# Kernel optimization log

Hardware: AMD Instinct MI355X
Metric: run time of the kernel (lower is better)

## Reference

```python
import jax, jax.numpy as jnp
import numpy as np

IN_CAPS, IN_SIZE = 1152, 8
OUT_CAPS, OUT_SIZE = 10, 16
NUM_ITERS = 3


def squash(s, axis=-1, eps=1e-8):
    sq = jnp.sum(s * s, axis=axis, keepdims=True)
    norm = jnp.sqrt(sq + eps)
    return (sq / (1.0 + sq)) * (s / norm)


def setup_inputs() -> dict:
    key = jax.random.key(0)
    kx, kw = jax.random.split(key)
    x = jax.random.normal(kx, (512, IN_CAPS, IN_SIZE), dtype=jnp.float32)
    W = jax.random.normal(kw, (IN_CAPS, OUT_CAPS, OUT_SIZE, IN_SIZE), dtype=jnp.float32)
    return {"x": x, "W": W}


def reference(x, W):
    # u_hat[b,i,o,p] = sum_q W[i,o,p,q] x[b,i,q]   -> [B, I, O, P]
    u_hat = jnp.einsum("iopq,biq->biop", W, x)
    b_ij = jnp.zeros((IN_CAPS, OUT_CAPS), dtype=u_hat.dtype)
    v_j = None
    for _ in range(NUM_ITERS):
        # legacy F.softmax on [1,I,O,1] with no dim -> softmax over dim=1 (in_capsules)
        c_ij = jax.nn.softmax(b_ij, axis=0)                      # [I, O]
        s_j = jnp.einsum("io,biop->bop", c_ij, u_hat)            # [B, O, P]
        v_j = squash(s_j, axis=-1)                               # [B, O, P]
        # agreement, averaged over batch
        u_vj1 = jnp.einsum("biop,bop->io", u_hat, v_j) / x.shape[0]
        b_ij = b_ij + u_vj1
    return v_j  # [B, 10, 16]
```

## Files before the change

kernel.cpp:

```cpp
#include <hip/hip_runtime.h>
#include <hip/hip_bf16.h>

#define B 512
#define IC 1152
#define QD 8
#define OD 10
#define PD 16
#define KD (IC * QD)
#define NKB (KD / 32)
#define NCS 72
#define KSTEPS (NKB / NCS)
#define NCB 4
#define SOP (B * OD * PD)
#define IO (IC * OD)
#define XE (B * KD)
#define PREPX (XE / 8 / 256)

typedef short bf16x8 __attribute__((ext_vector_type(8)));
typedef short bf16x4 __attribute__((ext_vector_type(4)));
typedef float f32x4 __attribute__((ext_vector_type(4)));

__device__ __forceinline__ short f2bf(float f) {
  union { float f; unsigned u; } x;
  x.f = f;
  unsigned r = x.u + 0x7FFFu + ((x.u >> 16) & 1u);
  return (short)(r >> 16);
}

__global__ __launch_bounds__(256) void prep_kernel(const float* __restrict__ x,
                                                   const float* __restrict__ W,
                                                   float* __restrict__ bijT,
                                                   short* __restrict__ Bs,
                                                   short* __restrict__ xB) {
  const int bid = blockIdx.x, tid = threadIdx.x;
  if (bid < PREPX) {
    const size_t e0 = (((size_t)bid << 8) + tid) * 8;
    const float4 a = *(const float4*)(x + e0);
    const float4 b = *(const float4*)(x + e0 + 4);
    short ov[8];
    ov[0] = f2bf(a.x); ov[1] = f2bf(a.y); ov[2] = f2bf(a.z); ov[3] = f2bf(a.w);
    ov[4] = f2bf(b.x); ov[5] = f2bf(b.y); ov[6] = f2bf(b.z); ov[7] = f2bf(b.w);
    *(int4*)(xB + e0) = *(const int4*)ov;
    return;
  }
  const int t = (bid - PREPX) * 256 + tid;
  if (t < IO) bijT[t] = 0.f;
  const int kb = t / 160, n = t % 160;
  const int o = n >> 4, p = n & 15;
  const float ci = 1.0f / (float)IC;
  short ov[32];
#pragma unroll
  for (int quad = 0; quad < 4; ++quad) {
    const int i = kb * 4 + quad;
    const float4* wp = (const float4*)(W + (((size_t)i * OD + o) * PD + p) * QD);
    const float4 w0 = wp[0], w1 = wp[1];
    ov[quad * 8 + 0] = f2bf(ci * w0.x); ov[quad * 8 + 1] = f2bf(ci * w0.y);
    ov[quad * 8 + 2] = f2bf(ci * w0.z); ov[quad * 8 + 3] = f2bf(ci * w0.w);
    ov[quad * 8 + 4] = f2bf(ci * w1.x); ov[quad * 8 + 5] = f2bf(ci * w1.y);
    ov[quad * 8 + 6] = f2bf(ci * w1.z); ov[quad * 8 + 7] = f2bf(ci * w1.w);
  }
  int4* dst = (int4*)(Bs + (size_t)t * 32);
  const int4* src = (const int4*)ov;
#pragma unroll
  for (int j = 0; j < 4; ++j) dst[j] = src[j];
}

__global__ __launch_bounds__(256) void rbn_kernel(const float* __restrict__ W,
                                                  const float* __restrict__ bijT,
                                                  short* __restrict__ Bs) {
  __shared__ float wred[4][OD];
  __shared__ float invs[OD];
  const int tid = threadIdx.x;
  const int wave = tid >> 6, lane = tid & 63;
  float lsum[OD];
#pragma unroll
  for (int o = 0; o < OD; ++o) lsum[o] = 0.f;
  for (int i = tid; i < IC; i += 256) {
#pragma unroll
    for (int o = 0; o < OD; ++o) lsum[o] += __expf(bijT[(size_t)o * IC + i]);
  }
#pragma unroll
  for (int o = 0; o < OD; ++o) {
    float s = lsum[o];
#pragma unroll
    for (int st = 1; st < 64; st <<= 1) s += __shfl_xor(s, st);
    if (lane == 0) wred[wave][o] = s;
  }
  __syncthreads();
  if (tid < OD)
    invs[tid] = 1.f / (wred[0][tid] + wred[1][tid] + wred[2][tid] + wred[3][tid]);
  __syncthreads();
  const int t = blockIdx.x * 256 + tid;
  const int kb = t / 160, n = t % 160;
  const int o = n >> 4, p = n & 15;
  const float inv = invs[o];
  const float4 bv = *(const float4*)(bijT + (size_t)o * IC + kb * 4);
  float cw[4];
  cw[0] = __expf(bv.x) * inv; cw[1] = __expf(bv.y) * inv;
  cw[2] = __expf(bv.z) * inv; cw[3] = __expf(bv.w) * inv;
  short ov[32];
#pragma unroll
  for (int quad = 0; quad < 4; ++quad) {
    const int i = kb * 4 + quad;
    const float ci = cw[quad];
    const float4* wp = (const float4*)(W + (((size_t)i * OD + o) * PD + p) * QD);
    const float4 w0 = wp[0], w1 = wp[1];
    ov[quad * 8 + 0] = f2bf(ci * w0.x); ov[quad * 8 + 1] = f2bf(ci * w0.y);
    ov[quad * 8 + 2] = f2bf(ci * w0.z); ov[quad * 8 + 3] = f2bf(ci * w0.w);
    ov[quad * 8 + 4] = f2bf(ci * w1.x); ov[quad * 8 + 5] = f2bf(ci * w1.y);
    ov[quad * 8 + 6] = f2bf(ci * w1.z); ov[quad * 8 + 7] = f2bf(ci * w1.w);
  }
  int4* dst = (int4*)(Bs + (size_t)t * 32);
  const int4* src = (const int4*)ov;
#pragma unroll
  for (int j = 0; j < 4; ++j) dst[j] = src[j];
}

__global__ __launch_bounds__(256) void sgemm_kernel(const short* __restrict__ xB,
                                                    const short* __restrict__ Bs,
                                                    float* __restrict__ s_part) {
  const int tid = threadIdx.x;
  const int wave = tid >> 6, lane = tid & 63;
  const int ln = lane & 15, quad = lane >> 4;
  const int cz = blockIdx.x % NCS, mb = blockIdx.x / NCS;
  const int m0 = mb * 64 + wave * 16;
  f32x4 acc[10] = {};
  const short* arow = xB + (size_t)(m0 + ln) * KD + quad * 8;
#pragma unroll
  for (int step = 0; step < KSTEPS; ++step) {
    const int kb = cz * KSTEPS + step;
    const bf16x8 af = *(const bf16x8*)(arow + kb * 32);
    const short* bp = Bs + (size_t)kb * 5120 + ln * 32 + quad * 8;
#pragma unroll
    for (int nt = 0; nt < 10; ++nt) {
      const bf16x8 bf = *(const bf16x8*)(bp + nt * 512);
      acc[nt] = __builtin_amdgcn_mfma_f32_16x16x32_bf16(af, bf, acc[nt], 0, 0, 0);
    }
  }
  float* sp = s_part + (size_t)cz * SOP;
#pragma unroll
  for (int nt = 0; nt < 10; ++nt)
#pragma unroll
    for (int r = 0; r < 4; ++r)
      sp[(size_t)(m0 + quad * 4 + r) * 160 + nt * 16 + ln] = acc[nt][r];
}

__global__ __launch_bounds__(256) void squash_kernel(const float* __restrict__ s_part,
                                                     short* __restrict__ vB,
                                                     float* __restrict__ out,
                                                     int write_out) {
  const int t = blockIdx.x * 256 + threadIdx.x;
  float sv = 0.f;
#pragma unroll 8
  for (int ch = 0; ch < NCS; ++ch) sv += s_part[(size_t)ch * SOP + t];
  float sq = sv * sv;
#pragma unroll
  for (int m = 1; m < 16; m <<= 1) sq += __shfl_xor(sq, m, 16);
  const float norm = sqrtf(sq + 1e-8f);
  const float val = sv * (sq / ((1.f + sq) * norm));
  if (write_out) {
    out[t] = val;
  } else {
    const int b = t / 160, n = t - b * 160;
    vB[((size_t)(b >> 5) * 160 + n) * 32 + (b & 31)] = f2bf(val);
  }
}

__global__ __launch_bounds__(256) void aggemm_kernel(const short* __restrict__ xB,
                                                     const float* __restrict__ W,
                                                     const short* __restrict__ vB,
                                                     float* __restrict__ bijT) {
  __shared__ __align__(16) short Abuf[16 * 64 * 8];
  const int tid = threadIdx.x;
  const int ig8 = blockIdx.x, kq = blockIdx.y;
  const int b0 = kq * 128;
#pragma unroll
  for (int j = 0; j < 8; ++j) {
    const int idx = tid + j * 256;
    const int b = idx >> 4, f4 = idx & 15;
    const bf16x4 vx = *(const bf16x4*)(xB + (size_t)(b0 + b) * KD + ig8 * 64 + f4 * 4);
    const int kb = b >> 5, qk = (b & 31) >> 3, jj = b & 7;
    const int mt2 = (f4 * 4) >> 4;
    const int mlb = (f4 & 3) * 4;
    short* dst = Abuf + (((mt2 * 4 + kb) * 64 + qk * 16 + mlb) * 8 + jj);
    dst[0] = vx[0]; dst[8] = vx[1]; dst[16] = vx[2]; dst[24] = vx[3];
  }
  __syncthreads();
  const int mt = tid >> 6, lane = tid & 63;
  const int ln = lane & 15, quad = lane >> 4;
  f32x4 acc[10] = {};
#pragma unroll
  for (int kb = 0; kb < 4; ++kb) {
    const bf16x8 af = *(const bf16x8*)(Abuf + ((mt * 4 + kb) * 64 + lane) * 8);
    const short* bp = vB + ((size_t)(kq * 4 + kb) * 160 + ln) * 32 + quad * 8;
#pragma unroll
    for (int nt = 0; nt < 10; ++nt) {
      const bf16x8 bf = *(const bf16x8*)(bp + nt * 512);
      acc[nt] = __builtin_amdgcn_mfma_f32_16x16x32_bf16(af, bf, acc[nt], 0, 0, 0);
    }
  }
  const int i = ig8 * 8 + mt * 2 + (quad >> 1);
  const int qb = (quad & 1) * 4;
#pragma unroll
  for (int nt = 0; nt < 10; ++nt) {
    const float4 wv = *(const float4*)(W + (((size_t)i * OD + nt) * PD + ln) * QD + qb);
    float pa = acc[nt][0] * wv.x + acc[nt][1] * wv.y + acc[nt][2] * wv.z + acc[nt][3] * wv.w;
    pa += __shfl_xor(pa, 1); pa += __shfl_xor(pa, 2); pa += __shfl_xor(pa, 4);
    pa += __shfl_xor(pa, 8); pa += __shfl_xor(pa, 16);
    if ((lane & 31) == 0)
      atomicAdd(&bijT[(size_t)nt * IC + i], pa * (1.0f / (float)B));
  }
}


extern "C" void kernel_launch(void* const* d_in, const int* in_sizes, int n_in,
                              void* d_out, int out_size, void* d_ws, size_t ws_size,
                              hipStream_t stream) {
  const float* x = (const float*)d_in[0];
  const float* W = (const float*)d_in[1];
  float* out = (float*)d_out;

  float* ws = (float*)d_ws;
  float* s_part = ws;
  float* bijT = s_part + (size_t)NCS * SOP;
  short* vB = (short*)(bijT + IO);
  short* Bs = vB + (size_t)16 * 160 * 32;
  short* xB = Bs + (size_t)NKB * 160 * 32;

  const dim3 agrid(144, NCB);

  prep_kernel<<<PREPX + 180, 256, 0, stream>>>(x, W, bijT, Bs, xB);
  sgemm_kernel<<<8 * NCS, 256, 0, stream>>>(xB, Bs, s_part);
  squash_kernel<<<SOP / 256, 256, 0, stream>>>(s_part, vB, out, 0);
  aggemm_kernel<<<agrid, 256, 0, stream>>>(xB, W, vB, bijT);
  rbn_kernel<<<180, 256, 0, stream>>>(W, bijT, Bs);
  sgemm_kernel<<<8 * NCS, 256, 0, stream>>>(xB, Bs, s_part);
  squash_kernel<<<SOP / 256, 256, 0, stream>>>(s_part, vB, out, 0);
  aggemm_kernel<<<agrid, 256, 0, stream>>>(xB, W, vB, bijT);
  rbn_kernel<<<180, 256, 0, stream>>>(W, bijT, Bs);
  sgemm_kernel<<<8 * NCS, 256, 0, stream>>>(xB, Bs, s_part);
  squash_kernel<<<SOP / 256, 256, 0, stream>>>(s_part, vB, out, 1);
}
```

Measured before the change: 177.7 us.

## Precompute transposed bf16 x once and halve sgemm K-split count

Result: no change. 178.1 us (+0.2%).

```diff
diff --git a/kernel.cpp b/kernel.cpp
--- a/kernel.cpp
+++ b/kernel.cpp
@@ -8,13 +8,12 @@
 #define PD 16
 #define KD (IC * QD)
 #define NKB (KD / 32)
-#define NCS 72
+#define NCS 36
 #define KSTEPS (NKB / NCS)
 #define NCB 4
 #define SOP (B * OD * PD)
 #define IO (IC * OD)
-#define XE (B * KD)
-#define PREPX (XE / 8 / 256)
+#define TPX ((B / 64) * (KD / 64))
 
 typedef short bf16x8 __attribute__((ext_vector_type(8)));
 typedef short bf16x4 __attribute__((ext_vector_type(4)));
@@ -31,19 +30,35 @@
                                                    const float* __restrict__ W,
                                                    float* __restrict__ bijT,
                                                    short* __restrict__ Bs,
-                                                   short* __restrict__ xB) {
+                                                   short* __restrict__ xB,
+                                                   short* __restrict__ xT) {
   const int bid = blockIdx.x, tid = threadIdx.x;
-  if (bid < PREPX) {
-    const size_t e0 = (((size_t)bid << 8) + tid) * 8;
-    const float4 a = *(const float4*)(x + e0);
-    const float4 b = *(const float4*)(x + e0 + 4);
-    short ov[8];
-    ov[0] = f2bf(a.x); ov[1] = f2bf(a.y); ov[2] = f2bf(a.z); ov[3] = f2bf(a.w);
-    ov[4] = f2bf(b.x); ov[5] = f2bf(b.y); ov[6] = f2bf(b.z); ov[7] = f2bf(b.w);
-    *(int4*)(xB + e0) = *(const int4*)ov;
+  if (bid < TPX) {
+    __shared__ short lds[64 * 72];
+    const int bt = bid / (KD / 64), qt = bid % (KD / 64);
+    const int b0 = bt * 64, c0 = qt * 64;
+    const int row0 = tid >> 4, col4 = (tid & 15) * 4;
+#pragma unroll
+    for (int j = 0; j < 4; ++j) {
+      const int row = row0 + j * 16;
+      const float4 v = *(const float4*)(x + (size_t)(b0 + row) * KD + c0 + col4);
+      bf16x4 ov;
+      ov[0] = f2bf(v.x); ov[1] = f2bf(v.y); ov[2] = f2bf(v.z); ov[3] = f2bf(v.w);
+      *(bf16x4*)(xB + (size_t)(b0 + row) * KD + c0 + col4) = ov;
+      lds[(col4 + 0) * 72 + row] = ov[0];
+      lds[(col4 + 1) * 72 + row] = ov[1];
+      lds[(col4 + 2) * 72 + row] = ov[2];
+      lds[(col4 + 3) * 72 + row] = ov[3];
+    }
+    __syncthreads();
+    const int iq = tid & 63, seg = tid >> 6;
+    const short* src = lds + iq * 72 + seg * 16;
+    short* dst = xT + (size_t)(c0 + iq) * B + b0 + seg * 16;
+    *(bf16x8*)dst = *(const bf16x8*)src;
+    *(bf16x8*)(dst + 8) = *(const bf16x8*)(src + 8);
     return;
   }
-  const int t = (bid - PREPX) * 256 + tid;
+  const int t = (bid - TPX) * 256 + tid;
   if (t < IO) bijT[t] = 0.f;
   const int kb = t / 160, n = t % 160;
   const int o = n >> 4, p = n & 15;
@@ -151,7 +166,7 @@
                                                      int write_out) {
   const int t = blockIdx.x * 256 + threadIdx.x;
   float sv = 0.f;
-#pragma unroll 8
+#pragma unroll 6
   for (int ch = 0; ch < NCS; ++ch) sv += s_part[(size_t)ch * SOP + t];
   float sq = sv * sv;
 #pragma unroll
@@ -166,32 +181,19 @@
   }
 }
 
-__global__ __launch_bounds__(256) void aggemm_kernel(const short* __restrict__ xB,
+__global__ __launch_bounds__(256) void aggemm_kernel(const short* __restrict__ xT,
                                                      const float* __restrict__ W,
                                                      const short* __restrict__ vB,
                                                      float* __restrict__ bijT) {
-  __shared__ __align__(16) short Abuf[16 * 64 * 8];
   const int tid = threadIdx.x;
   const int ig8 = blockIdx.x, kq = blockIdx.y;
-  const int b0 = kq * 128;
-#pragma unroll
-  for (int j = 0; j < 8; ++j) {
-    const int idx = tid + j * 256;
-    const int b = idx >> 4, f4 = idx & 15;
-    const bf16x4 vx = *(const bf16x4*)(xB + (size_t)(b0 + b) * KD + ig8 * 64 + f4 * 4);
-    const int kb = b >> 5, qk = (b & 31) >> 3, jj = b & 7;
-    const int mt2 = (f4 * 4) >> 4;
-    const int mlb = (f4 & 3) * 4;
-    short* dst = Abuf + (((mt2 * 4 + kb) * 64 + qk * 16 + mlb) * 8 + jj);
-    dst[0] = vx[0]; dst[8] = vx[1]; dst[16] = vx[2]; dst[24] = vx[3];
-  }
-  __syncthreads();
   const int mt = tid >> 6, lane = tid & 63;
   const int ln = lane & 15, quad = lane >> 4;
   f32x4 acc[10] = {};
+  const short* arow = xT + (size_t)(ig8 * 64 + mt * 16 + ln) * B + kq * 128 + quad * 8;
 #pragma unroll
   for (int kb = 0; kb < 4; ++kb) {
-    const bf16x8 af = *(const bf16x8*)(Abuf + ((mt * 4 + kb) * 64 + lane) * 8);
+    const bf16x8 af = *(const bf16x8*)(arow + kb * 32);
     const short* bp = vB + ((size_t)(kq * 4 + kb) * 160 + ln) * 32 + quad * 8;
 #pragma unroll
     for (int nt = 0; nt < 10; ++nt) {
@@ -226,17 +228,18 @@
   short* vB = (short*)(bijT + IO);
   short* Bs = vB + (size_t)16 * 160 * 32;
   short* xB = Bs + (size_t)NKB * 160 * 32;
+  short* xT = xB + (size_t)B * KD;
 
   const dim3 agrid(144, NCB);
 
-  prep_kernel<<<PREPX + 180, 256, 0, stream>>>(x, W, bijT, Bs, xB);
+  prep_kernel<<<TPX + 180, 256, 0, stream>>>(x, W, bijT, Bs, xB, xT);
   sgemm_kernel<<<8 * NCS, 256, 0, stream>>>(xB, Bs, s_part);
   squash_kernel<<<SOP / 256, 256, 0, stream>>>(s_part, vB, out, 0);
-  aggemm_kernel<<<agrid, 256, 0, stream>>>(xB, W, vB, bijT);
+  aggemm_kernel<<<agrid, 256, 0, stream>>>(xT, W, vB, bijT);
   rbn_kernel<<<180, 256, 0, stream>>>(W, bijT, Bs);
   sgemm_kernel<<<8 * NCS, 256, 0, stream>>>(xB, Bs, s_part);
   squash_kernel<<<SOP / 256, 256, 0, stream>>>(s_part, vB, out, 0);
-  aggemm_kernel<<<agrid, 256, 0, stream>>>(xB, W, vB, bijT);
+  aggemm_kernel<<<agrid, 256, 0, stream>>>(xT, W, vB, bijT);
   rbn_kernel<<<180, 256, 0, stream>>>(W, bijT, Bs);
   sgemm_kernel<<<8 * NCS, 256, 0, stream>>>(xB, Bs, s_part);
   squash_kernel<<<SOP / 256, 256, 0, stream>>>(s_part, vB, out, 1);
```
